# Optimization experiments

Measured on AMD Instinct MI355X. Metric: run time of the kernel, lower is better.

## Reference

```python
import jax, jax.numpy as jnp
import numpy as np

B, P, C, H, W = 2048, 50, 512, 7, 8


def setup_inputs() -> dict:
    key = jax.random.key(0)
    k1, k2 = jax.random.split(key)
    x = jax.random.normal(k1, (B, C, H, W), dtype=jnp.float32)
    # nn.init.xavier_uniform_ on (P, C, H, W) -> small-scale init
    prototype = jax.random.normal(k2, (P, C, H, W), dtype=jnp.float32) * 0.02
    return {"x": x, "prototype": prototype}


def reference(x, prototype):
    """PrototypeLayer euclidean branch.

    Torch original:
      x2_sum = conv2d(x**2, ones_like(prototype))   # full-size kernel -> [B,P,1,1], same value per p
      p2     = sum(prototype**2, dims=(1,2,3)).view(1,P,1,1)
      xp     = conv2d(x, prototype)                  # [B,P,1,1]
      dist   = relu(x2_sum + p2 - 2*xp).view(B,P)
    The full-size-kernel convs reduce to global sums / a [B,P] contraction.
    """
    x2_sum = jnp.sum(x * x, axis=(1, 2, 3))                 # [B]
    p2 = jnp.sum(prototype * prototype, axis=(1, 2, 3))     # [P]
    xp = jnp.einsum('bchw,pchw->bp', x, prototype)          # [B,P]
    distance = jax.nn.relu(x2_sum[:, None] + p2[None, :] - 2.0 * xp)
    return distance
```

## Files before the change

kernel.cpp:

```cpp
#include <hip/hip_runtime.h>
#include <hip/hip_bf16.h>


typedef __bf16 bf16_t;
typedef bf16_t bf16x8 __attribute__((ext_vector_type(8)));
typedef bf16_t bf16x4 __attribute__((ext_vector_type(4)));
typedef float  floatx4 __attribute__((ext_vector_type(4)));

#define KDIM 28672
#define BDIM 2048
#define KSPLIT 16
#define KCHUNK (KDIM / KSPLIT)
#define ITERS (KCHUNK / 64)
#define LDS_STRIDE 72

__global__ __launch_bounds__(256) void proto_prep(const float* __restrict__ proto,
                                                  bf16_t* __restrict__ pb,
                                                  float* __restrict__ p2) {
    int p = blockIdx.x;
    int t = threadIdx.x;
    float acc = 0.f;
    if (p < 50) {
        const floatx4* src = (const floatx4*)(proto + (long)p * KDIM);
        for (int i = t; i < KDIM / 4; i += 256) {
            floatx4 v = src[i];
            acc += v[0]*v[0] + v[1]*v[1] + v[2]*v[2] + v[3]*v[3];
            bf16x4 o;
            o[0] = (bf16_t)v[0]; o[1] = (bf16_t)v[1];
            o[2] = (bf16_t)v[2]; o[3] = (bf16_t)v[3];
            *(bf16x4*)(pb + (long)p * KDIM + i * 4) = o;
        }
    } else {
        bf16x4 z;
        z[0] = (bf16_t)0.f; z[1] = (bf16_t)0.f; z[2] = (bf16_t)0.f; z[3] = (bf16_t)0.f;
        for (int i = t; i < KDIM / 4; i += 256)
            *(bf16x4*)(pb + (long)p * KDIM + i * 4) = z;
    }
    __shared__ float sred[256];
    sred[t] = acc;
    __syncthreads();
    for (int s = 128; s > 0; s >>= 1) {
        if (t < s) sred[t] += sred[t + s];
        __syncthreads();
    }
    if (t == 0) p2[p] = (p < 50) ? sred[0] : 0.f;
}

__global__ __launch_bounds__(256, 2) void proto_main(const float* __restrict__ x,
                                                     const bf16_t* __restrict__ pb,
                                                     float* __restrict__ xpp,
                                                     float* __restrict__ x2p) {
    __shared__ bf16_t As[64 * LDS_STRIDE];
    __shared__ bf16_t Bs[64 * LDS_STRIDE];

    const int t = threadIdx.x;
    const int mbase = blockIdx.x * 64;
    const int ks = blockIdx.y;
    const int kbase0 = ks * KCHUNK;

    const int row = t >> 2;
    const int q = t & 3;
    const float* xrow = x + (long)(mbase + row) * KDIM + kbase0 + q * 16;
    const bf16_t* prow = pb + (long)row * KDIM + kbase0 + q * 16;
    bf16_t* aw = As + row * LDS_STRIDE + q * 16;
    bf16_t* bw = Bs + row * LDS_STRIDE + q * 16;

    const int lane = t & 63;
    const int wave = t >> 6;
    const int m0 = (wave >> 1) * 32;
    const int n0 = (wave & 1) * 32;
    const int lr = lane & 15;
    const int lk = (lane >> 4) * 8;

    floatx4 acc00 = {0.f, 0.f, 0.f, 0.f};
    floatx4 acc01 = {0.f, 0.f, 0.f, 0.f};
    floatx4 acc10 = {0.f, 0.f, 0.f, 0.f};
    floatx4 acc11 = {0.f, 0.f, 0.f, 0.f};
    float x2acc = 0.f;

    for (int it = 0; it < ITERS; ++it) {
        const int kb = it * 64;
        floatx4 v0 = *(const floatx4*)(xrow + kb);
        floatx4 v1 = *(const floatx4*)(xrow + kb + 4);
        floatx4 v2 = *(const floatx4*)(xrow + kb + 8);
        floatx4 v3 = *(const floatx4*)(xrow + kb + 12);
        bf16x8 pv0 = ((const bf16x8*)(prow + kb))[0];
        bf16x8 pv1 = ((const bf16x8*)(prow + kb))[1];

        x2acc += v0[0]*v0[0] + v0[1]*v0[1] + v0[2]*v0[2] + v0[3]*v0[3]
               + v1[0]*v1[0] + v1[1]*v1[1] + v1[2]*v1[2] + v1[3]*v1[3]
               + v2[0]*v2[0] + v2[1]*v2[1] + v2[2]*v2[2] + v2[3]*v2[3]
               + v3[0]*v3[0] + v3[1]*v3[1] + v3[2]*v3[2] + v3[3]*v3[3];
        bf16x8 lo, hi;
        lo[0] = (bf16_t)v0[0]; lo[1] = (bf16_t)v0[1]; lo[2] = (bf16_t)v0[2]; lo[3] = (bf16_t)v0[3];
        lo[4] = (bf16_t)v1[0]; lo[5] = (bf16_t)v1[1]; lo[6] = (bf16_t)v1[2]; lo[7] = (bf16_t)v1[3];
        hi[0] = (bf16_t)v2[0]; hi[1] = (bf16_t)v2[1]; hi[2] = (bf16_t)v2[2]; hi[3] = (bf16_t)v2[3];
        hi[4] = (bf16_t)v3[0]; hi[5] = (bf16_t)v3[1]; hi[6] = (bf16_t)v3[2]; hi[7] = (bf16_t)v3[3];

        __syncthreads();
        *(bf16x8*)aw       = lo;
        *(bf16x8*)(aw + 8) = hi;
        *(bf16x8*)bw       = pv0;
        *(bf16x8*)(bw + 8) = pv1;
        __syncthreads();

        #pragma unroll
        for (int kk = 0; kk < 64; kk += 32) {
            bf16x8 a0 = *(const bf16x8*)(As + (m0 + lr) * LDS_STRIDE + kk + lk);
            bf16x8 a1 = *(const bf16x8*)(As + (m0 + 16 + lr) * LDS_STRIDE + kk + lk);
            bf16x8 b0 = *(const bf16x8*)(Bs + (n0 + lr) * LDS_STRIDE + kk + lk);
            bf16x8 b1 = *(const bf16x8*)(Bs + (n0 + 16 + lr) * LDS_STRIDE + kk + lk);
            acc00 = __builtin_amdgcn_mfma_f32_16x16x32_bf16(a0, b0, acc00, 0, 0, 0);
            acc01 = __builtin_amdgcn_mfma_f32_16x16x32_bf16(a0, b1, acc01, 0, 0, 0);
            acc10 = __builtin_amdgcn_mfma_f32_16x16x32_bf16(a1, b0, acc10, 0, 0, 0);
            acc11 = __builtin_amdgcn_mfma_f32_16x16x32_bf16(a1, b1, acc11, 0, 0, 0);
        }
    }

    const long base = ((long)ks * BDIM + mbase) * 64;
    const int nn = lane & 15;
    #pragma unroll
    for (int r = 0; r < 4; ++r) {
        const int ml = m0 + (lane >> 4) * 4 + r;
        xpp[base + (long)ml * 64 + n0 + nn]             = acc00[r];
        xpp[base + (long)ml * 64 + n0 + 16 + nn]        = acc01[r];
        xpp[base + (long)(ml + 16) * 64 + n0 + nn]      = acc10[r];
        xpp[base + (long)(ml + 16) * 64 + n0 + 16 + nn] = acc11[r];
    }

    __syncthreads();
    float* red = (float*)As;
    red[t] = x2acc;
    __syncthreads();
    if (t < 64) {
        float s = red[4 * t] + red[4 * t + 1] + red[4 * t + 2] + red[4 * t + 3];
        x2p[ks * BDIM + mbase + t] = s;
    }
}

__global__ __launch_bounds__(256) void proto_finalize(const float* __restrict__ xpp,
                                                      const float* __restrict__ x2p,
                                                      const float* __restrict__ p2,
                                                      float* __restrict__ out) {
    int idx = blockIdx.x * 256 + threadIdx.x;
    int b = idx >> 6;
    int n = idx & 63;
    if (n >= 50) return;
    float xp = 0.f, x2 = 0.f;
    #pragma unroll
    for (int ksi = 0; ksi < KSPLIT; ++ksi) {
        xp += xpp[((long)ksi * BDIM + b) * 64 + n];
        x2 += x2p[ksi * BDIM + b];
    }
    float d = x2 + p2[n] - 2.f * xp;
    out[b * 50 + n] = d > 0.f ? d : 0.f;
}

extern "C" void kernel_launch(void* const* d_in, const int* in_sizes, int n_in,
                              void* d_out, int out_size, void* d_ws, size_t ws_size,
                              hipStream_t stream) {
    const float* x = (const float*)d_in[0];
    const float* proto = (const float*)d_in[1];
    float* out = (float*)d_out;

    char* ws = (char*)d_ws;
    bf16_t* pb  = (bf16_t*)(ws);
    float*  p2  = (float*)(ws + 3670016);
    float*  x2p = (float*)(ws + 3670272);
    float*  xpp = (float*)(ws + 3801344);

    proto_prep<<<64, 256, 0, stream>>>(proto, pb, p2);
    proto_main<<<dim3(32, KSPLIT), 256, 0, stream>>>(x, pb, xpp, x2p);
    proto_finalize<<<(BDIM * 64) / 256, 256, 0, stream>>>(xpp, x2p, p2, out);
}
```

Measured before the change: 341.2 us.

## Load MFMA operands directly from global with register prefetch, drop LDS staging

The main GEMM kernel stops staging x and prototype tiles through shared memory. Each wave now loads its own 16-row slice of x and all 64 prototype rows straight into MFMA operand registers, with a one-step register prefetch. The K split doubles to 32 and the occupancy hint rises to 4 blocks per CU, to put more blocks in flight on this bandwidth-bound x stream. In exchange, each block rereads the prototype matrix once per wave instead of sharing it, and the split-K partial buffer and the finalize reduction double in size.

```diff
diff --git a/kernel.cpp b/kernel.cpp
--- a/kernel.cpp
+++ b/kernel.cpp
@@ -9,10 +9,9 @@
 
 #define KDIM 28672
 #define BDIM 2048
-#define KSPLIT 16
+#define KSPLIT 32
 #define KCHUNK (KDIM / KSPLIT)
-#define ITERS (KCHUNK / 64)
-#define LDS_STRIDE 72
+#define STEPS (KCHUNK / 32)
 
 __global__ __launch_bounds__(256) void proto_prep(const float* __restrict__ proto,
                                                   bf16_t* __restrict__ pb,
@@ -46,95 +45,78 @@
     if (t == 0) p2[p] = (p < 50) ? sred[0] : 0.f;
 }
 
-__global__ __launch_bounds__(256, 2) void proto_main(const float* __restrict__ x,
+__global__ __launch_bounds__(256, 4) void proto_main(const float* __restrict__ x,
                                                      const bf16_t* __restrict__ pb,
                                                      float* __restrict__ xpp,
                                                      float* __restrict__ x2p) {
-    __shared__ bf16_t As[64 * LDS_STRIDE];
-    __shared__ bf16_t Bs[64 * LDS_STRIDE];
-
     const int t = threadIdx.x;
+    const int lane = t & 63;
+    const int wave = t >> 6;
+    const int lr = lane & 15;
+    const int quad = lane >> 4;
     const int mbase = blockIdx.x * 64;
     const int ks = blockIdx.y;
-    const int kbase0 = ks * KCHUNK;
+    const int kbase = ks * KCHUNK;
 
-    const int row = t >> 2;
-    const int q = t & 3;
-    const float* xrow = x + (long)(mbase + row) * KDIM + kbase0 + q * 16;
-    const bf16_t* prow = pb + (long)row * KDIM + kbase0 + q * 16;
-    bf16_t* aw = As + row * LDS_STRIDE + q * 16;
-    bf16_t* bw = Bs + row * LDS_STRIDE + q * 16;
+    const int mrow = mbase + wave * 16 + lr;
+    const float* xr = x + (long)mrow * KDIM + kbase + quad * 8;
+    const bf16_t* pr0 = pb + (long)(0  + lr) * KDIM + kbase + quad * 8;
+    const bf16_t* pr1 = pb + (long)(16 + lr) * KDIM + kbase + quad * 8;
+    const bf16_t* pr2 = pb + (long)(32 + lr) * KDIM + kbase + quad * 8;
+    const bf16_t* pr3 = pb + (long)(48 + lr) * KDIM + kbase + quad * 8;
 
-    const int lane = t & 63;
-    const int wave = t >> 6;
-    const int m0 = (wave >> 1) * 32;
-    const int n0 = (wave & 1) * 32;
-    const int lr = lane & 15;
-    const int lk = (lane >> 4) * 8;
-
-    floatx4 acc00 = {0.f, 0.f, 0.f, 0.f};
-    floatx4 acc01 = {0.f, 0.f, 0.f, 0.f};
-    floatx4 acc10 = {0.f, 0.f, 0.f, 0.f};
-    floatx4 acc11 = {0.f, 0.f, 0.f, 0.f};
+    floatx4 acc0 = {0.f,0.f,0.f,0.f};
+    floatx4 acc1 = {0.f,0.f,0.f,0.f};
+    floatx4 acc2 = {0.f,0.f,0.f,0.f};
+    floatx4 acc3 = {0.f,0.f,0.f,0.f};
     float x2acc = 0.f;
 
-    for (int it = 0; it < ITERS; ++it) {
-        const int kb = it * 64;
-        floatx4 v0 = *(const floatx4*)(xrow + kb);
-        floatx4 v1 = *(const floatx4*)(xrow + kb + 4);
-        floatx4 v2 = *(const floatx4*)(xrow + kb + 8);
-        floatx4 v3 = *(const floatx4*)(xrow + kb + 12);
-        bf16x8 pv0 = ((const bf16x8*)(prow + kb))[0];
-        bf16x8 pv1 = ((const bf16x8*)(prow + kb))[1];
+    floatx4 a0 = *(const floatx4*)(xr);
+    floatx4 a1 = *(const floatx4*)(xr + 4);
+    bf16x8 b0 = *(const bf16x8*)(pr0);
+    bf16x8 b1 = *(const bf16x8*)(pr1);
+    bf16x8 b2 = *(const bf16x8*)(pr2);
+    bf16x8 b3 = *(const bf16x8*)(pr3);
 
-        x2acc += v0[0]*v0[0] + v0[1]*v0[1] + v0[2]*v0[2] + v0[3]*v0[3]
-               + v1[0]*v1[0] + v1[1]*v1[1] + v1[2]*v1[2] + v1[3]*v1[3]
-               + v2[0]*v2[0] + v2[1]*v2[1] + v2[2]*v2[2] + v2[3]*v2[3]
-               + v3[0]*v3[0] + v3[1]*v3[1] + v3[2]*v3[2] + v3[3]*v3[3];
-        bf16x8 lo, hi;
-        lo[0] = (bf16_t)v0[0]; lo[1] = (bf16_t)v0[1]; lo[2] = (bf16_t)v0[2]; lo[3] = (bf16_t)v0[3];
-        lo[4] = (bf16_t)v1[0]; lo[5] = (bf16_t)v1[1]; lo[6] = (bf16_t)v1[2]; lo[7] = (bf16_t)v1[3];
-        hi[0] = (bf16_t)v2[0]; hi[1] = (bf16_t)v2[1]; hi[2] = (bf16_t)v2[2]; hi[3] = (bf16_t)v2[3];
-        hi[4] = (bf16_t)v3[0]; hi[5] = (bf16_t)v3[1]; hi[6] = (bf16_t)v3[2]; hi[7] = (bf16_t)v3[3];
+    for (int it = 0; it < STEPS; ++it) {
+        const int nk = (it + 1 < STEPS ? it + 1 : 0) * 32;
+        floatx4 na0 = *(const floatx4*)(xr + nk);
+        floatx4 na1 = *(const floatx4*)(xr + nk + 4);
+        bf16x8 nb0 = *(const bf16x8*)(pr0 + nk);
+        bf16x8 nb1 = *(const bf16x8*)(pr1 + nk);
+        bf16x8 nb2 = *(const bf16x8*)(pr2 + nk);
+        bf16x8 nb3 = *(const bf16x8*)(pr3 + nk);
 
-        __syncthreads();
-        *(bf16x8*)aw       = lo;
-        *(bf16x8*)(aw + 8) = hi;
-        *(bf16x8*)bw       = pv0;
-        *(bf16x8*)(bw + 8) = pv1;
-        __syncthreads();
+        x2acc += a0[0]*a0[0] + a0[1]*a0[1] + a0[2]*a0[2] + a0[3]*a0[3]
+               + a1[0]*a1[0] + a1[1]*a1[1] + a1[2]*a1[2] + a1[3]*a1[3];
+        bf16x8 av;
+        av[0] = (bf16_t)a0[0]; av[1] = (bf16_t)a0[1];
+        av[2] = (bf16_t)a0[2]; av[3] = (bf16_t)a0[3];
+        av[4] = (bf16_t)a1[0]; av[5] = (bf16_t)a1[1];
+        av[6] = (bf16_t)a1[2]; av[7] = (bf16_t)a1[3];
 
-        #pragma unroll
-        for (int kk = 0; kk < 64; kk += 32) {
-            bf16x8 a0 = *(const bf16x8*)(As + (m0 + lr) * LDS_STRIDE + kk + lk);
-            bf16x8 a1 = *(const bf16x8*)(As + (m0 + 16 + lr) * LDS_STRIDE + kk + lk);
-            bf16x8 b0 = *(const bf16x8*)(Bs + (n0 + lr) * LDS_STRIDE + kk + lk);
-            bf16x8 b1 = *(const bf16x8*)(Bs + (n0 + 16 + lr) * LDS_STRIDE + kk + lk);
-            acc00 = __builtin_amdgcn_mfma_f32_16x16x32_bf16(a0, b0, acc00, 0, 0, 0);
-            acc01 = __builtin_amdgcn_mfma_f32_16x16x32_bf16(a0, b1, acc01, 0, 0, 0);
-            acc10 = __builtin_amdgcn_mfma_f32_16x16x32_bf16(a1, b0, acc10, 0, 0, 0);
-            acc11 = __builtin_amdgcn_mfma_f32_16x16x32_bf16(a1, b1, acc11, 0, 0, 0);
-        }
+        acc0 = __builtin_amdgcn_mfma_f32_16x16x32_bf16(av, b0, acc0, 0, 0, 0);
+        acc1 = __builtin_amdgcn_mfma_f32_16x16x32_bf16(av, b1, acc1, 0, 0, 0);
+        acc2 = __builtin_amdgcn_mfma_f32_16x16x32_bf16(av, b2, acc2, 0, 0, 0);
+        acc3 = __builtin_amdgcn_mfma_f32_16x16x32_bf16(av, b3, acc3, 0, 0, 0);
+
+        a0 = na0; a1 = na1;
+        b0 = nb0; b1 = nb1; b2 = nb2; b3 = nb3;
     }
 
-    const long base = ((long)ks * BDIM + mbase) * 64;
-    const int nn = lane & 15;
+    x2acc += __shfl_xor(x2acc, 16, 64);
+    x2acc += __shfl_xor(x2acc, 32, 64);
+    if (quad == 0)
+        x2p[ks * BDIM + mbase + wave * 16 + lr] = x2acc;
+
+    const long base = ((long)ks * BDIM + mbase + wave * 16) * 64;
     #pragma unroll
     for (int r = 0; r < 4; ++r) {
-        const int ml = m0 + (lane >> 4) * 4 + r;
-        xpp[base + (long)ml * 64 + n0 + nn]             = acc00[r];
-        xpp[base + (long)ml * 64 + n0 + 16 + nn]        = acc01[r];
-        xpp[base + (long)(ml + 16) * 64 + n0 + nn]      = acc10[r];
-        xpp[base + (long)(ml + 16) * 64 + n0 + 16 + nn] = acc11[r];
-    }
-
-    __syncthreads();
-    float* red = (float*)As;
-    red[t] = x2acc;
-    __syncthreads();
-    if (t < 64) {
-        float s = red[4 * t] + red[4 * t + 1] + red[4 * t + 2] + red[4 * t + 3];
-        x2p[ks * BDIM + mbase + t] = s;
+        const int mr = quad * 4 + r;
+        xpp[base + (long)mr * 64 + 0  + lr] = acc0[r];
+        xpp[base + (long)mr * 64 + 16 + lr] = acc1[r];
+        xpp[base + (long)mr * 64 + 32 + lr] = acc2[r];
+        xpp[base + (long)mr * 64 + 48 + lr] = acc3[r];
     }
 }
 
@@ -167,7 +149,7 @@
     bf16_t* pb  = (bf16_t*)(ws);
     float*  p2  = (float*)(ws + 3670016);
     float*  x2p = (float*)(ws + 3670272);
-    float*  xpp = (float*)(ws + 3801344);
+    float*  xpp = (float*)(ws + 3932416);
 
     proto_prep<<<64, 256, 0, stream>>>(proto, pb, p2);
     proto_main<<<dim3(32, KSPLIT), 256, 0, stream>>>(x, pb, xpp, x2p);
```

Measured after the change: 366.5 us. 1.07x slower.
